# Kernel optimization log

Measured on AMD Instinct MI355X. Metric: run time of the kernel, lower is better.

## Reference

```python
import jax, jax.numpy as jnp
import numpy as np

VOCAB = 100000
EDIM = 300
MUS = np.array([-0.9, -0.7, -0.5, -0.3, -0.1, 0.1, 0.3, 0.5, 0.7, 0.9, 1.0], dtype=np.float32)
SIGMAS = np.array([0.1] * 10 + [0.001], dtype=np.float32)


def setup_inputs() -> dict:
    key = jax.random.key(0)
    k1, k2, k3, k4, k5, k6 = jax.random.split(key, 6)
    B, Q, D = 128, 16, 1024
    doctoks = jax.random.randint(k1, (B, D), 0, VOCAB)
    querytoks = jax.random.randint(k2, (B, Q), 0, VOCAB)
    query_idf = jax.random.uniform(k3, (B, Q), dtype=jnp.float32)
    emb_table = jax.random.normal(k4, (VOCAB, EDIM), dtype=jnp.float32) * 0.1
    # pad token 0 -> zero embedding (padding_idx semantics)
    emb_table = emb_table.at[0].set(0.0)
    mus = jnp.asarray(MUS)
    sigmas = jnp.asarray(SIGMAS)
    K = mus.shape[0]
    fc_w = jax.random.normal(k5, (1, K), dtype=jnp.float32) * (1.0 / np.sqrt(K))
    fc_b = jax.random.normal(k6, (1,), dtype=jnp.float32) * 0.01
    return {"doctoks": doctoks, "querytoks": querytoks, "query_idf": query_idf,
            "emb_table": emb_table, "mus": mus, "sigmas": sigmas,
            "fc_w": fc_w, "fc_b": fc_b}


def reference(doctoks, querytoks, query_idf, emb_table, mus, sigmas, fc_w, fc_b):
    eps = 1e-9
    q_emb = emb_table[querytoks]                # [B,Q,E]
    d_emb = emb_table[doctoks]                  # [B,D,E]
    qn = q_emb / (jnp.linalg.norm(q_emb, axis=-1, keepdims=True) + eps)
    dn = d_emb / (jnp.linalg.norm(d_emb, axis=-1, keepdims=True) + eps)
    simmat = jnp.einsum('bqe,bde->bqd', qn, dn)  # cosine sim [B,Q,D]
    # zero out padded positions (token id 0)
    pad_mask = (querytoks != 0)[:, :, None] & (doctoks != 0)[:, None, :]
    simmat = jnp.where(pad_mask, simmat, 0.0)
    # RBF kernel bank broadcast at dim=1: [B,K,Q,D]
    diff = simmat[:, None, :, :] - mus[None, :, None, None]
    kernels = jnp.exp(-0.5 * diff * diff / (sigmas[None, :, None, None] ** 2))
    result = kernels.sum(axis=3)                 # [B,K,Q]
    mask = (simmat.sum(axis=2) != 0.0)[:, None, :]  # [B,1,Q] -> broadcasts over K
    mask = jnp.broadcast_to(mask, result.shape)
    result = jnp.where(mask, jnp.log(result + 1e-6), 0.0)
    result = result.sum(axis=2)                  # [B,K]
    scores = result @ fc_w.T + fc_b              # [B,1]
    return scores
```

## Files before the change

### kernel.cpp

```cpp
#include <hip/hip_runtime.h>

#define EDIM 300
#define NB   128
#define NQ   16
#define ND   1024
#define NK   11
#define BLOCK 128
#define MDOC  4
#define DOCS_PER_BLOCK (BLOCK * MDOC)
#define BLOCKS_PER_B   2
#define NCHUNK 75
#define SIMW (DOCS_PER_BLOCK + 4)

__global__ __launch_bounds__(BLOCK) void knrm_main(
    const int*   __restrict__ dtoks,
    const int*   __restrict__ qtoks,
    const float* __restrict__ emb,
    const float* __restrict__ mus,
    const float* __restrict__ sigmas,
    float*       __restrict__ part) {
    __shared__ __align__(16) float qn_s[NQ * EDIM];
    __shared__ __align__(16) float sim_t[NQ * SIMW];
    __shared__ float rs_s[NQ];
    __shared__ float red_s[NK * NQ * 8];

    const int blk  = blockIdx.x;
    const int b    = blk >> 1;
    const int half = blk & 1;
    const int tid  = threadIdx.x;

    for (int i = tid; i < NQ * EDIM; i += BLOCK) {
        int q = i / EDIM;
        int e = i - q * EDIM;
        qn_s[i] = emb[(size_t)qtoks[b * NQ + q] * EDIM + e];
    }
    __syncthreads();
    {
        int q = tid >> 3, j = tid & 7;
        float ss = 0.f;
        for (int e = j; e < EDIM; e += 8) { float v = qn_s[q * EDIM + e]; ss += v * v; }
        ss += __shfl_xor(ss, 1, 64);
        ss += __shfl_xor(ss, 2, 64);
        ss += __shfl_xor(ss, 4, 64);
        if (j == 0) rs_s[q] = 1.0f / (sqrtf(ss) + 1e-9f);
    }
    __syncthreads();
    for (int i = tid; i < NQ * EDIM; i += BLOCK) qn_s[i] *= rs_s[i / EDIM];
    __syncthreads();

    const int d0 = half * DOCS_PER_BLOCK + tid * MDOC;
    int4 tks = *(const int4*)&dtoks[b * ND + d0];
    const float4* rp0 = (const float4*)(emb + (size_t)tks.x * EDIM);
    const float4* rp1 = (const float4*)(emb + (size_t)tks.y * EDIM);
    const float4* rp2 = (const float4*)(emb + (size_t)tks.z * EDIM);
    const float4* rp3 = (const float4*)(emb + (size_t)tks.w * EDIM);

    float sims[MDOC][NQ];
#pragma unroll
    for (int m = 0; m < MDOC; ++m)
#pragma unroll
        for (int q = 0; q < NQ; ++q) sims[m][q] = 0.f;
    float ssq0 = 0.f, ssq1 = 0.f, ssq2 = 0.f, ssq3 = 0.f;

    float4 a0 = rp0[0], a1 = rp1[0], a2 = rp2[0], a3 = rp3[0];

#define KNRM_BODY(CIDX)                                                        \
    do {                                                                       \
        ssq0 += a0.x*a0.x + a0.y*a0.y + a0.z*a0.z + a0.w*a0.w;                 \
        ssq1 += a1.x*a1.x + a1.y*a1.y + a1.z*a1.z + a1.w*a1.w;                 \
        ssq2 += a2.x*a2.x + a2.y*a2.y + a2.z*a2.z + a2.w*a2.w;                 \
        ssq3 += a3.x*a3.x + a3.y*a3.y + a3.z*a3.z + a3.w*a3.w;                 \
        const float* qb = qn_s + (CIDX) * 4;                                   \
        _Pragma("unroll")                                                      \
        for (int q = 0; q < NQ; ++q) {                                         \
            float4 qv = *(const float4*)(qb + q * EDIM);        \
            sims[0][q] += qv.x*a0.x + qv.y*a0.y + qv.z*a0.z + qv.w*a0.w;       \
            sims[1][q] += qv.x*a1.x + qv.y*a1.y + qv.z*a1.z + qv.w*a1.w;       \
            sims[2][q] += qv.x*a2.x + qv.y*a2.y + qv.z*a2.z + qv.w*a2.w;       \
            sims[3][q] += qv.x*a3.x + qv.y*a3.y + qv.z*a3.z + qv.w*a3.w;       \
        }                                                                      \
    } while (0)

    for (int c = 0; c < NCHUNK - 1; ++c) {
        float4 n0 = rp0[c + 1], n1 = rp1[c + 1], n2 = rp2[c + 1], n3 = rp3[c + 1];
        KNRM_BODY(c);
        a0 = n0; a1 = n1; a2 = n2; a3 = n3;
    }
    KNRM_BODY(NCHUNK - 1);
#undef KNRM_BODY

    float rn0 = 1.0f / (sqrtf(ssq0) + 1e-9f);
    float rn1 = 1.0f / (sqrtf(ssq1) + 1e-9f);
    float rn2 = 1.0f / (sqrtf(ssq2) + 1e-9f);
    float rn3 = 1.0f / (sqrtf(ssq3) + 1e-9f);

#pragma unroll
    for (int q = 0; q < NQ; ++q) {
        *(float4*)&sim_t[q * SIMW + tid * 4] =
            make_float4(sims[0][q]*rn0, sims[1][q]*rn1, sims[2][q]*rn2, sims[3][q]*rn3);
    }
    __syncthreads();

    {
        const int q = tid & 15;
        const int s = tid >> 4;
        float mu[NK], cc[NK], acc[NK];
#pragma unroll
        for (int k = 0; k < NK; ++k) {
            mu[k] = mus[k];
            float sg = sigmas[k];
            cc[k] = -0.5f / (sg * sg);
            acc[k] = 0.f;
        }
        const float* row = sim_t + q * SIMW + s * 64;
        for (int i = 0; i < 16; ++i) {
            float4 s4 = *(const float4*)(row + i * 4);
#pragma unroll
            for (int k = 0; k < NK; ++k) {
                float e0 = s4.x - mu[k], e1 = s4.y - mu[k];
                float e2 = s4.z - mu[k], e3 = s4.w - mu[k];
                acc[k] += __expf(cc[k]*e0*e0) + __expf(cc[k]*e1*e1)
                        + __expf(cc[k]*e2*e2) + __expf(cc[k]*e3*e3);
            }
        }
#pragma unroll
        for (int k = 0; k < NK; ++k) red_s[(k * NQ + q) * 8 + s] = acc[k];
    }
    __syncthreads();

    for (int t = tid; t < NK * NQ; t += BLOCK) {
        float r = 0.f;
#pragma unroll
        for (int j = 0; j < 8; ++j) r += red_s[t * 8 + j];
        part[blk * (NK * NQ) + t] = r;
    }
}

__global__ void knrm_final(const float* __restrict__ part,
                           const int*   __restrict__ qtoks,
                           const float* __restrict__ fc_w,
                           const float* __restrict__ fc_b,
                           float*       __restrict__ out) {
    __shared__ float red[NK * NQ];
    __shared__ float ks[NK];
    int b = blockIdx.x;
    int t = threadIdx.x;
    if (t < NK * NQ) {
        int q = t & 15;
        float r = 0.f;
        for (int j = 0; j < BLOCKS_PER_B; ++j)
            r += part[(b * BLOCKS_PER_B + j) * (NK * NQ) + t];
        red[t] = (qtoks[b * NQ + q] != 0) ? logf(r + 1e-6f) : 0.f;
    }
    __syncthreads();
    if (t < NK) {
        float s = 0.f;
        for (int q = 0; q < NQ; ++q) s += red[t * NQ + q];
        ks[t] = s * fc_w[t];
    }
    __syncthreads();
    if (t == 0) {
        float s = fc_b[0];
        for (int k = 0; k < NK; ++k) s += ks[k];
        out[b] = s;
    }
}

extern "C" void kernel_launch(void* const* d_in, const int* in_sizes, int n_in,
                              void* d_out, int out_size, void* d_ws, size_t ws_size,
                              hipStream_t stream) {
    const int*   doctoks   = (const int*)  d_in[0];
    const int*   querytoks = (const int*)  d_in[1];
    const float* emb       = (const float*)d_in[3];
    const float* mus       = (const float*)d_in[4];
    const float* sigmas    = (const float*)d_in[5];
    const float* fc_w      = (const float*)d_in[6];
    const float* fc_b      = (const float*)d_in[7];
    float* out = (float*)d_out;

    float* part = (float*)d_ws;

    knrm_main<<<NB * BLOCKS_PER_B, BLOCK, 0, stream>>>(doctoks, querytoks, emb,
                                                       mus, sigmas, part);
    knrm_final<<<NB, 192, 0, stream>>>(part, querytoks, fc_w, fc_b, out);
}
```

Before: 248.2 us.

## Precompute normalized queries and split docs and embedding dim across more blocks

Adds a separate kernel that normalizes query embeddings once into workspace, so the main kernel no longer stages them in shared memory. The main kernel now uses 8 blocks per batch with 2 docs per thread, and its two waves each take half of the embedding dimension, reducing partial sims through shared memory. This raises block count from 256 to 1024 to fill the GPU better and cuts register and LDS pressure. In exchange, query vectors are read from global/L2 on every chunk, and there is an extra launch plus a cross-wave reduction.

```diff
diff --git a/kernel.cpp b/kernel.cpp
--- a/kernel.cpp
+++ b/kernel.cpp
@@ -6,98 +6,110 @@
 #define ND   1024
 #define NK   11
 #define BLOCK 128
-#define MDOC  4
-#define DOCS_PER_BLOCK (BLOCK * MDOC)
-#define BLOCKS_PER_B   2
-#define NCHUNK 75
-#define SIMW (DOCS_PER_BLOCK + 4)
+#define MDOC  2
+#define DOCS_PER_BLOCK 128
+#define BLOCKS_PER_B   8
+#define Q4STRIDE 75
+#define PW 132
+
+__global__ void qnorm_kernel(const int* __restrict__ qtoks,
+                             const float* __restrict__ emb,
+                             float* __restrict__ qn) {
+    int row  = blockIdx.x;
+    int lane = threadIdx.x;
+    int tok  = qtoks[row];
+    const float* src = emb + (size_t)tok * EDIM;
+    float v[5];
+    float ssq = 0.f;
+#pragma unroll
+    for (int j = 0; j < 5; ++j) {
+        int e = lane + 64 * j;
+        v[j] = (e < EDIM) ? src[e] : 0.f;
+        ssq += v[j] * v[j];
+    }
+#pragma unroll
+    for (int off = 32; off >= 1; off >>= 1)
+        ssq += __shfl_xor(ssq, off, 64);
+    float rn = 1.0f / (sqrtf(ssq) + 1e-9f);
+#pragma unroll
+    for (int j = 0; j < 5; ++j) {
+        int e = lane + 64 * j;
+        if (e < EDIM) qn[(size_t)row * EDIM + e] = v[j] * rn;
+    }
+}
 
 __global__ __launch_bounds__(BLOCK) void knrm_main(
     const int*   __restrict__ dtoks,
-    const int*   __restrict__ qtoks,
     const float* __restrict__ emb,
+    const float* __restrict__ qn,
     const float* __restrict__ mus,
     const float* __restrict__ sigmas,
     float*       __restrict__ part) {
-    __shared__ __align__(16) float qn_s[NQ * EDIM];
-    __shared__ __align__(16) float sim_t[NQ * SIMW];
-    __shared__ float rs_s[NQ];
+    __shared__ __align__(16) float psim[NQ * PW];
+    __shared__ float pssq[PW];
     __shared__ float red_s[NK * NQ * 8];
 
-    const int blk  = blockIdx.x;
-    const int b    = blk >> 1;
-    const int half = blk & 1;
-    const int tid  = threadIdx.x;
-
-    for (int i = tid; i < NQ * EDIM; i += BLOCK) {
-        int q = i / EDIM;
-        int e = i - q * EDIM;
-        qn_s[i] = emb[(size_t)qtoks[b * NQ + q] * EDIM + e];
+    const int blk   = blockIdx.x;
+    const int b     = blk >> 3;
+    const int dbase = (blk & 7) * DOCS_PER_BLOCK;
+    const int tid   = threadIdx.x;
+    const int lane  = tid & 63;
+    const int w     = tid >> 6;
+    const int c0    = w ? 38 : 0;
+    const int nch   = w ? 37 : 38;
+
+    const int d0 = dbase + lane * MDOC;
+    int2 tks = *(const int2*)&dtoks[b * ND + d0];
+    const float4* dp0 = (const float4*)(emb + (size_t)tks.x * EDIM) + c0;
+    const float4* dp1 = (const float4*)(emb + (size_t)tks.y * EDIM) + c0;
+    const float4* qp  = (const float4*)(qn) + (size_t)b * NQ * Q4STRIDE + c0;
+
+    float sims[MDOC][NQ];
+#pragma unroll
+    for (int m = 0; m < MDOC; ++m)
+#pragma unroll
+        for (int q = 0; q < NQ; ++q) sims[m][q] = 0.f;
+    float ssq0 = 0.f, ssq1 = 0.f;
+
+    float4 a0 = dp0[0], a1 = dp1[0];
+    for (int c = 0; c < nch; ++c) {
+        int cn = (c + 1 < nch) ? c + 1 : c;
+        float4 n0 = dp0[cn], n1 = dp1[cn];
+        ssq0 += a0.x*a0.x + a0.y*a0.y + a0.z*a0.z + a0.w*a0.w;
+        ssq1 += a1.x*a1.x + a1.y*a1.y + a1.z*a1.z + a1.w*a1.w;
+#pragma unroll
+        for (int q = 0; q < NQ; ++q) {
+            float4 qv = qp[q * Q4STRIDE + c];
+            sims[0][q] += qv.x*a0.x + qv.y*a0.y + qv.z*a0.z + qv.w*a0.w;
+            sims[1][q] += qv.x*a1.x + qv.y*a1.y + qv.z*a1.z + qv.w*a1.w;
+        }
+        a0 = n0; a1 = n1;
+    }
+
+    if (w == 0) {
+#pragma unroll
+        for (int q = 0; q < NQ; ++q) {
+            psim[q * PW + lane * 2]     = sims[0][q];
+            psim[q * PW + lane * 2 + 1] = sims[1][q];
+        }
+        pssq[lane * 2]     = ssq0;
+        pssq[lane * 2 + 1] = ssq1;
+    }
+    __syncthreads();
+    if (w == 1) {
+#pragma unroll
+        for (int q = 0; q < NQ; ++q) {
+            psim[q * PW + lane * 2]     += sims[0][q];
+            psim[q * PW + lane * 2 + 1] += sims[1][q];
+        }
+        pssq[lane * 2]     += ssq0;
+        pssq[lane * 2 + 1] += ssq1;
     }
     __syncthreads();
     {
-        int q = tid >> 3, j = tid & 7;
-        float ss = 0.f;
-        for (int e = j; e < EDIM; e += 8) { float v = qn_s[q * EDIM + e]; ss += v * v; }
-        ss += __shfl_xor(ss, 1, 64);
-        ss += __shfl_xor(ss, 2, 64);
-        ss += __shfl_xor(ss, 4, 64);
-        if (j == 0) rs_s[q] = 1.0f / (sqrtf(ss) + 1e-9f);
-    }
-    __syncthreads();
-    for (int i = tid; i < NQ * EDIM; i += BLOCK) qn_s[i] *= rs_s[i / EDIM];
-    __syncthreads();
-
-    const int d0 = half * DOCS_PER_BLOCK + tid * MDOC;
-    int4 tks = *(const int4*)&dtoks[b * ND + d0];
-    const float4* rp0 = (const float4*)(emb + (size_t)tks.x * EDIM);
-    const float4* rp1 = (const float4*)(emb + (size_t)tks.y * EDIM);
-    const float4* rp2 = (const float4*)(emb + (size_t)tks.z * EDIM);
-    const float4* rp3 = (const float4*)(emb + (size_t)tks.w * EDIM);
-
-    float sims[MDOC][NQ];
-#pragma unroll
-    for (int m = 0; m < MDOC; ++m)
-#pragma unroll
-        for (int q = 0; q < NQ; ++q) sims[m][q] = 0.f;
-    float ssq0 = 0.f, ssq1 = 0.f, ssq2 = 0.f, ssq3 = 0.f;
-
-    float4 a0 = rp0[0], a1 = rp1[0], a2 = rp2[0], a3 = rp3[0];
-
-#define KNRM_BODY(CIDX)                                                        \
-    do {                                                                       \
-        ssq0 += a0.x*a0.x + a0.y*a0.y + a0.z*a0.z + a0.w*a0.w;                 \
-        ssq1 += a1.x*a1.x + a1.y*a1.y + a1.z*a1.z + a1.w*a1.w;                 \
-        ssq2 += a2.x*a2.x + a2.y*a2.y + a2.z*a2.z + a2.w*a2.w;                 \
-        ssq3 += a3.x*a3.x + a3.y*a3.y + a3.z*a3.z + a3.w*a3.w;                 \
-        const float* qb = qn_s + (CIDX) * 4;                                   \
-        _Pragma("unroll")                                                      \
-        for (int q = 0; q < NQ; ++q) {                                         \
-            float4 qv = *(const float4*)(qb + q * EDIM);        \
-            sims[0][q] += qv.x*a0.x + qv.y*a0.y + qv.z*a0.z + qv.w*a0.w;       \
-            sims[1][q] += qv.x*a1.x + qv.y*a1.y + qv.z*a1.z + qv.w*a1.w;       \
-            sims[2][q] += qv.x*a2.x + qv.y*a2.y + qv.z*a2.z + qv.w*a2.w;       \
-            sims[3][q] += qv.x*a3.x + qv.y*a3.y + qv.z*a3.z + qv.w*a3.w;       \
-        }                                                                      \
-    } while (0)
-
-    for (int c = 0; c < NCHUNK - 1; ++c) {
-        float4 n0 = rp0[c + 1], n1 = rp1[c + 1], n2 = rp2[c + 1], n3 = rp3[c + 1];
-        KNRM_BODY(c);
-        a0 = n0; a1 = n1; a2 = n2; a3 = n3;
-    }
-    KNRM_BODY(NCHUNK - 1);
-#undef KNRM_BODY
-
-    float rn0 = 1.0f / (sqrtf(ssq0) + 1e-9f);
-    float rn1 = 1.0f / (sqrtf(ssq1) + 1e-9f);
-    float rn2 = 1.0f / (sqrtf(ssq2) + 1e-9f);
-    float rn3 = 1.0f / (sqrtf(ssq3) + 1e-9f);
-
-#pragma unroll
-    for (int q = 0; q < NQ; ++q) {
-        *(float4*)&sim_t[q * SIMW + tid * 4] =
-            make_float4(sims[0][q]*rn0, sims[1][q]*rn1, sims[2][q]*rn2, sims[3][q]*rn3);
+        float rn = 1.0f / (sqrtf(pssq[tid]) + 1e-9f);
+#pragma unroll
+        for (int q = 0; q < NQ; ++q) psim[q * PW + tid] *= rn;
     }
     __syncthreads();
 
@@ -112,8 +124,9 @@
             cc[k] = -0.5f / (sg * sg);
             acc[k] = 0.f;
         }
-        const float* row = sim_t + q * SIMW + s * 64;
-        for (int i = 0; i < 16; ++i) {
+        const float* row = psim + q * PW + s * 16;
+#pragma unroll
+        for (int i = 0; i < 4; ++i) {
             float4 s4 = *(const float4*)(row + i * 4);
 #pragma unroll
             for (int k = 0; k < NK; ++k) {
@@ -178,9 +191,11 @@
     const float* fc_b      = (const float*)d_in[7];
     float* out = (float*)d_out;
 
-    float* part = (float*)d_ws;
-
-    knrm_main<<<NB * BLOCKS_PER_B, BLOCK, 0, stream>>>(doctoks, querytoks, emb,
+    float* qn   = (float*)d_ws;
+    float* part = qn + (size_t)NB * NQ * EDIM;
+
+    qnorm_kernel<<<NB * NQ, 64, 0, stream>>>(querytoks, emb, qn);
+    knrm_main<<<NB * BLOCKS_PER_B, BLOCK, 0, stream>>>(doctoks, emb, qn,
                                                        mus, sigmas, part);
     knrm_final<<<NB, 192, 0, stream>>>(part, querytoks, fc_w, fc_b, out);
 }
```

Result: slower. 389.3 us (+56.9%).

## Stage doc embeddings through coalesced shared-memory panels and split queries across waves

Applied to the files above, without the earlier changes.

Instead of each thread gathering four full embedding rows with strided per-thread float4 loads, the block cooperatively loads 32-float column panels of 256 document rows into padded shared memory with coalesced accesses. Each of the two waves then computes similarities for half the queries over all 256 docs. The grid doubles to four blocks per batch item. This is meant to improve global-load coalescing and occupancy, but it adds ten barrier-separated panel stages and leaves the next panel's loads unoverlapped with compute.

```diff
diff --git a/kernel.cpp b/kernel.cpp
--- a/kernel.cpp
+++ b/kernel.cpp
@@ -7,10 +7,11 @@
 #define NK   11
 #define BLOCK 128
 #define MDOC  4
-#define DOCS_PER_BLOCK (BLOCK * MDOC)
-#define BLOCKS_PER_B   2
-#define NCHUNK 75
-#define SIMW (DOCS_PER_BLOCK + 4)
+#define TDOCS 256
+#define BLOCKS_PER_B 4
+#define NPANEL 10
+#define PPITCH 36
+#define SIMP 260
 
 __global__ __launch_bounds__(BLOCK) void knrm_main(
     const int*   __restrict__ dtoks,
@@ -20,18 +21,22 @@
     const float* __restrict__ sigmas,
     float*       __restrict__ part) {
     __shared__ __align__(16) float qn_s[NQ * EDIM];
-    __shared__ __align__(16) float sim_t[NQ * SIMW];
+    __shared__ __align__(16) float panel[TDOCS * PPITCH];
+    __shared__ int   dtok_s[TDOCS];
     __shared__ float rs_s[NQ];
+    __shared__ __align__(16) float sim_t[NQ * SIMP];
     __shared__ float red_s[NK * NQ * 8];
 
-    const int blk  = blockIdx.x;
-    const int b    = blk >> 1;
-    const int half = blk & 1;
-    const int tid  = threadIdx.x;
+    const int blk   = blockIdx.x;
+    const int b     = blk >> 2;
+    const int dbase = (blk & 3) * TDOCS;
+    const int tid   = threadIdx.x;
+    const int lane  = tid & 63;
+    const int w     = tid >> 6;
 
+    for (int i = tid; i < TDOCS; i += BLOCK) dtok_s[i] = dtoks[b * ND + dbase + i];
     for (int i = tid; i < NQ * EDIM; i += BLOCK) {
-        int q = i / EDIM;
-        int e = i - q * EDIM;
+        int q = i / EDIM, e = i - q * EDIM;
         qn_s[i] = emb[(size_t)qtoks[b * NQ + q] * EDIM + e];
     }
     __syncthreads();
@@ -46,85 +51,83 @@
     }
     __syncthreads();
     for (int i = tid; i < NQ * EDIM; i += BLOCK) qn_s[i] *= rs_s[i / EDIM];
-    __syncthreads();
 
-    const int d0 = half * DOCS_PER_BLOCK + tid * MDOC;
-    int4 tks = *(const int4*)&dtoks[b * ND + d0];
-    const float4* rp0 = (const float4*)(emb + (size_t)tks.x * EDIM);
-    const float4* rp1 = (const float4*)(emb + (size_t)tks.y * EDIM);
-    const float4* rp2 = (const float4*)(emb + (size_t)tks.z * EDIM);
-    const float4* rp3 = (const float4*)(emb + (size_t)tks.w * EDIM);
-
-    float sims[MDOC][NQ];
+    float sims[MDOC][8];
 #pragma unroll
     for (int m = 0; m < MDOC; ++m)
 #pragma unroll
-        for (int q = 0; q < NQ; ++q) sims[m][q] = 0.f;
-    float ssq0 = 0.f, ssq1 = 0.f, ssq2 = 0.f, ssq3 = 0.f;
+        for (int qq = 0; qq < 8; ++qq) sims[m][qq] = 0.f;
+    float ssq[MDOC] = {0.f, 0.f, 0.f, 0.f};
 
-    float4 a0 = rp0[0], a1 = rp1[0], a2 = rp2[0], a3 = rp3[0];
+    const int s  = tid & 7;
+    const int r0 = tid >> 3;
 
-#define KNRM_BODY(CIDX)                                                        \
-    do {                                                                       \
-        ssq0 += a0.x*a0.x + a0.y*a0.y + a0.z*a0.z + a0.w*a0.w;                 \
-        ssq1 += a1.x*a1.x + a1.y*a1.y + a1.z*a1.z + a1.w*a1.w;                 \
-        ssq2 += a2.x*a2.x + a2.y*a2.y + a2.z*a2.z + a2.w*a2.w;                 \
-        ssq3 += a3.x*a3.x + a3.y*a3.y + a3.z*a3.z + a3.w*a3.w;                 \
-        const float* qb = qn_s + (CIDX) * 4;                                   \
-        _Pragma("unroll")                                                      \
-        for (int q = 0; q < NQ; ++q) {                                         \
-            float4 qv = *(const float4*)(qb + q * EDIM);        \
-            sims[0][q] += qv.x*a0.x + qv.y*a0.y + qv.z*a0.z + qv.w*a0.w;       \
-            sims[1][q] += qv.x*a1.x + qv.y*a1.y + qv.z*a1.z + qv.w*a1.w;       \
-            sims[2][q] += qv.x*a2.x + qv.y*a2.y + qv.z*a2.z + qv.w*a2.w;       \
-            sims[3][q] += qv.x*a3.x + qv.y*a3.y + qv.z*a3.z + qv.w*a3.w;       \
-        }                                                                      \
-    } while (0)
-
-    for (int c = 0; c < NCHUNK - 1; ++c) {
-        float4 n0 = rp0[c + 1], n1 = rp1[c + 1], n2 = rp2[c + 1], n3 = rp3[c + 1];
-        KNRM_BODY(c);
-        a0 = n0; a1 = n1; a2 = n2; a3 = n3;
+    for (int p = 0; p < NPANEL; ++p) {
+        __syncthreads();
+        if (p < 9 || s < 3) {
+#pragma unroll
+            for (int j = 0; j < 16; ++j) {
+                int r = r0 + 16 * j;
+                const float* src = emb + (size_t)dtok_s[r] * EDIM + p * 32 + s * 4;
+                *(float4*)&panel[r * PPITCH + s * 4] = *(const float4*)src;
+            }
+        }
+        __syncthreads();
+        const int cmax = (p == 9) ? 3 : 8;
+        for (int cc = 0; cc < cmax; ++cc) {
+            float4 dv[MDOC];
+#pragma unroll
+            for (int m = 0; m < MDOC; ++m)
+                dv[m] = *(const float4*)&panel[(lane + 64 * m) * PPITCH + cc * 4];
+#pragma unroll
+            for (int m = 0; m < MDOC; ++m)
+                ssq[m] += dv[m].x*dv[m].x + dv[m].y*dv[m].y + dv[m].z*dv[m].z + dv[m].w*dv[m].w;
+            const float* qb = qn_s + (size_t)w * 8 * EDIM + (p * 8 + cc) * 4;
+#pragma unroll
+            for (int qq = 0; qq < 8; ++qq) {
+                float4 qv = *(const float4*)(qb + qq * EDIM);
+#pragma unroll
+                for (int m = 0; m < MDOC; ++m) {
+                    sims[m][qq] += qv.x*dv[m].x + qv.y*dv[m].y + qv.z*dv[m].z + qv.w*dv[m].w;
+                }
+            }
+        }
     }
-    KNRM_BODY(NCHUNK - 1);
-#undef KNRM_BODY
-
-    float rn0 = 1.0f / (sqrtf(ssq0) + 1e-9f);
-    float rn1 = 1.0f / (sqrtf(ssq1) + 1e-9f);
-    float rn2 = 1.0f / (sqrtf(ssq2) + 1e-9f);
-    float rn3 = 1.0f / (sqrtf(ssq3) + 1e-9f);
 
 #pragma unroll
-    for (int q = 0; q < NQ; ++q) {
-        *(float4*)&sim_t[q * SIMW + tid * 4] =
-            make_float4(sims[0][q]*rn0, sims[1][q]*rn1, sims[2][q]*rn2, sims[3][q]*rn3);
+    for (int m = 0; m < MDOC; ++m) {
+        float rn = 1.0f / (sqrtf(ssq[m]) + 1e-9f);
+#pragma unroll
+        for (int qq = 0; qq < 8; ++qq)
+            sim_t[(w * 8 + qq) * SIMP + lane + 64 * m] = sims[m][qq] * rn;
     }
     __syncthreads();
 
     {
         const int q = tid & 15;
-        const int s = tid >> 4;
-        float mu[NK], cc[NK], acc[NK];
+        const int sl = tid >> 4;
+        float mu[NK], cc2[NK], acc[NK];
 #pragma unroll
         for (int k = 0; k < NK; ++k) {
             mu[k] = mus[k];
             float sg = sigmas[k];
-            cc[k] = -0.5f / (sg * sg);
+            cc2[k] = -0.5f / (sg * sg);
             acc[k] = 0.f;
         }
-        const float* row = sim_t + q * SIMW + s * 64;
-        for (int i = 0; i < 16; ++i) {
+        const float* row = sim_t + q * SIMP + sl * 32;
+#pragma unroll
+        for (int i = 0; i < 8; ++i) {
             float4 s4 = *(const float4*)(row + i * 4);
 #pragma unroll
             for (int k = 0; k < NK; ++k) {
                 float e0 = s4.x - mu[k], e1 = s4.y - mu[k];
                 float e2 = s4.z - mu[k], e3 = s4.w - mu[k];
-                acc[k] += __expf(cc[k]*e0*e0) + __expf(cc[k]*e1*e1)
-                        + __expf(cc[k]*e2*e2) + __expf(cc[k]*e3*e3);
+                acc[k] += __expf(cc2[k]*e0*e0) + __expf(cc2[k]*e1*e1)
+                        + __expf(cc2[k]*e2*e2) + __expf(cc2[k]*e3*e3);
             }
         }
 #pragma unroll
-        for (int k = 0; k < NK; ++k) red_s[(k * NQ + q) * 8 + s] = acc[k];
+        for (int k = 0; k < NK; ++k) red_s[(k * NQ + q) * 8 + sl] = acc[k];
     }
     __syncthreads();
 
```

Result: faster. 222.4 us (-10.4%).
